# Performance work log

Hardware: AMD Instinct MI355X
Metric: run time of the kernel (lower is better)

Reference implementation:

```python
import jax, jax.numpy as jnp
import numpy as np

GROUPS = 32
EPS = 1e-5


def setup_inputs() -> dict:
    key = jax.random.key(0)
    ks = jax.random.split(key, 7)
    B, C, H, W = 16, 512, 32, 32
    return {
        "x": jax.random.normal(ks[0], (B, C, H, W), jnp.float32),
        "norm_w": jax.random.uniform(ks[1], (C,), jnp.float32, 0.5, 1.5),
        "norm_b": jax.random.normal(ks[2], (C,), jnp.float32) * 0.1,
        "qkv_w": jax.random.normal(ks[3], (3 * C, C), jnp.float32) * (C ** -0.5),
        "qkv_b": jax.random.normal(ks[4], (3 * C,), jnp.float32) * 0.01,
        "proj_w": jax.random.normal(ks[5], (C, C), jnp.float32) * (C ** -0.5),
        "proj_b": jax.random.normal(ks[6], (C,), jnp.float32) * 0.01,
        "num_heads": 8,
    }


def _group_norm(x, w, b):
    # x: (B, C, T); GroupNorm over (C//G, T) per group, per-channel affine
    B, C, T = x.shape
    xg = x.reshape(B, GROUPS, C // GROUPS, T)
    mean = jnp.mean(xg, axis=(2, 3), keepdims=True)
    var = jnp.var(xg, axis=(2, 3), keepdims=True)
    xn = ((xg - mean) * jax.lax.rsqrt(var + EPS)).reshape(B, C, T)
    return xn * w[None, :, None] + b[None, :, None]


def reference(x, norm_w, norm_b, qkv_w, qkv_b, proj_w, proj_b, num_heads):
    B, C, H, W = x.shape
    T = H * W
    xf = x.reshape(B, C, T)
    # qkv conv1x1: (B, 3C, T)
    qkv = jnp.einsum('oc,bct->bot', qkv_w, _group_norm(xf, norm_w, norm_b)) \
        + qkv_b[None, :, None]
    # split heads: (B*H, 3*hd, T) then chunk on channel dim
    BH = B * num_heads
    qkv = qkv.reshape(BH, 3 * C // num_heads, T)
    q, k, v = jnp.split(qkv, 3, axis=1)  # each (BH, hd, T)
    hd = C // num_heads
    scale = hd ** -0.25
    # scores (BH, T, T), softmax in fp32 then cast back (matches torch)
    scores = jnp.einsum('bct,bcs->bts', q * scale, k * scale)
    w = jax.nn.softmax(scores.astype(jnp.float32), axis=-1).astype(scores.dtype)
    h = jnp.einsum('bts,bcs->bct', w, v)  # (BH, hd, T)
    h = h.reshape(B, C, T)
    h = jnp.einsum('oc,bct->bot', proj_w, h) + proj_b[None, :, None]
    return (h + xf).reshape(B, C, H, W)
```

## Files before the change

kernel.cpp:

```cpp
#include <hip/hip_runtime.h>

typedef unsigned short u16;
typedef unsigned int u32;
typedef __bf16 bf16x8 __attribute__((ext_vector_type(8)));
typedef float f32x4 __attribute__((ext_vector_type(4)));
typedef float f32x16 __attribute__((ext_vector_type(16)));

#define SCALE_QK 0.35355339059327373f
#define LOG2E 1.4426950408889634f

__device__ __forceinline__ u16 f2bf(float f) {
  u32 u = __float_as_uint(f);
  u += 0x7FFFu + ((u >> 16) & 1u);
  return (u16)(u >> 16);
}

__device__ __forceinline__ void gload16(const u16* g, u16* l) {
  __builtin_amdgcn_global_load_lds((const __attribute__((address_space(1))) void*)g,
                                   (__attribute__((address_space(3))) void*)l, 16, 0, 0);
}

__device__ __forceinline__ int rswz(int r) { return (r & 7) ^ ((r >> 3) & 3); }

__global__ __launch_bounds__(256) void k_prep(const float* __restrict__ x,
                                              const float* __restrict__ nw,
                                              const float* __restrict__ nb,
                                              const float* __restrict__ qkvw_f,
                                              const float* __restrict__ projw_f,
                                              u16* __restrict__ gnt,
                                              u16* __restrict__ qkvw,
                                              u16* __restrict__ projw) {
  const int bid = blockIdx.x;
  const int tid = threadIdx.x;

  if (bid >= 512) {
    const float* src = (bid < 1280) ? qkvw_f : projw_f;
    u16* dst = (bid < 1280) ? qkvw : projw;
    const int i = (bid - ((bid < 1280) ? 512 : 1280)) * 256 + tid;
    float4 v = ((const float4*)src)[i];
    u32 lo = (u32)f2bf(v.x) | ((u32)f2bf(v.y) << 16);
    u32 hi = (u32)f2bf(v.z) | ((u32)f2bf(v.w) << 16);
    ((uint2*)dst)[i] = make_uint2(lo, hi);
    return;
  }

  const int b = bid >> 5;
  const int g = bid & 31;
  const float* xg = x + ((size_t)b * 512 + g * 16) * 1024;

  float s = 0.f, ss = 0.f;
#pragma unroll
  for (int it = 0; it < 16; ++it) {
    float4 v = ((const float4*)xg)[tid + it * 256];
    s += v.x + v.y + v.z + v.w;
    ss += v.x * v.x + v.y * v.y + v.z * v.z + v.w * v.w;
  }
#pragma unroll
  for (int off = 32; off >= 1; off >>= 1) {
    s += __shfl_xor(s, off);
    ss += __shfl_xor(ss, off);
  }
  __shared__ float red[8];
  const int wid = tid >> 6, lane = tid & 63;
  if (lane == 0) { red[wid] = s; red[4 + wid] = ss; }
  __syncthreads();
  const float mean = (red[0] + red[1] + red[2] + red[3]) * (1.f / 16384.f);
  const float ex2 = (red[4] + red[5] + red[6] + red[7]) * (1.f / 16384.f);
  const float rstd = rsqrtf(ex2 - mean * mean + 1e-5f);

  const int cp = (tid & 7) * 2, tt = tid >> 3;
  const int c0 = g * 16 + cp;
  const float wc0 = nw[c0] * rstd, bc0 = nb[c0] - mean * wc0;
  const float wc1 = nw[c0 + 1] * rstd, bc1 = nb[c0 + 1] - mean * wc1;
  const float* xc0 = xg + (size_t)cp * 1024;
  const float* xc1 = xc0 + 1024;
  u16* dst = gnt + (size_t)b * 1024 * 512 + c0;
#pragma unroll 8
  for (int t = tt; t < 1024; t += 32) {
    const u32 v0 = f2bf(xc0[t] * wc0 + bc0);
    const u32 v1 = f2bf(xc1[t] * wc1 + bc1);
    *(u32*)(dst + (size_t)t * 512) = v0 | (v1 << 16);
  }
}

template <int MODE>
__global__ __launch_bounds__(512) void k_gemm(const u16* __restrict__ A,
                                              const u16* __restrict__ Bw,
                                              const float* __restrict__ bias,
                                              u16* __restrict__ Qb, u16* __restrict__ Kb,
                                              u16* __restrict__ Vb,
                                              const float* __restrict__ xres,
                                              float* __restrict__ out) {
  __shared__ u16 smem[32768];
  u16* Asb = smem;
  u16* Bsb = smem + 16384;
  const int tid = threadIdx.x;
  const int lane = tid & 63, wid = tid >> 6;
  const int wr = wid >> 1, wc = wid & 1;
  const int fid = blockIdx.x;
  const int m0 = (fid & 127) * 128;
  const int n0 = (fid >> 7) * 128;
  const int l15 = lane & 15, l4 = lane >> 4;
  const f32x4 fzero = {0.f, 0.f, 0.f, 0.f};

  f32x4 acc[2][4];
#pragma unroll
  for (int i = 0; i < 2; ++i)
#pragma unroll
    for (int j = 0; j < 4; ++j) acc[i][j] = fzero;

  const int lrow = (tid & 63) >> 3;
  const int lchunk = tid & 7;

  auto stage = [&](int bi, int kt) {
#pragma unroll
    for (int rd = 0; rd < 2; ++rd) {
      const int rbase = wid * 8 + rd * 64;
      const int r = rbase + lrow;
      const int q = lchunk ^ (r & 7);
      gload16(A + ((size_t)(m0 + r) * 512 + kt * 64 + q * 8), Asb + bi * 8192 + rbase * 64);
      gload16(Bw + ((size_t)(n0 + r) * 512 + kt * 64 + q * 8), Bsb + bi * 8192 + rbase * 64);
    }
  };

  stage(0, 0);
  stage(1, 1);

  for (int kt = 0; kt < 8; ++kt) {
    if (kt < 7) {
      asm volatile("s_waitcnt vmcnt(4)" ::: "memory");
    } else {
      asm volatile("s_waitcnt vmcnt(0)" ::: "memory");
    }
    __builtin_amdgcn_s_barrier();
    const int buf = kt & 1;
#pragma unroll
    for (int ks = 0; ks < 2; ++ks) {
      bf16x8 af[2], bfr[4];
#pragma unroll
      for (int mi = 0; mi < 2; ++mi) {
        const int row = wr * 32 + mi * 16 + l15;
        af[mi] = *(const bf16x8*)&Asb[buf * 8192 + row * 64 + (((((ks << 2) + l4)) ^ (row & 7)) << 3)];
      }
#pragma unroll
      for (int ni = 0; ni < 4; ++ni) {
        const int row = wc * 64 + ni * 16 + l15;
        bfr[ni] = *(const bf16x8*)&Bsb[buf * 8192 + row * 64 + (((((ks << 2) + l4)) ^ (row & 7)) << 3)];
      }
#pragma unroll
      for (int mi = 0; mi < 2; ++mi)
#pragma unroll
        for (int ni = 0; ni < 4; ++ni)
          acc[mi][ni] = __builtin_amdgcn_mfma_f32_16x16x32_bf16(af[mi], bfr[ni], acc[mi][ni], 0, 0, 0);
    }
    asm volatile("s_waitcnt lgkmcnt(0)" ::: "memory");
    __builtin_amdgcn_sched_barrier(0);
    __builtin_amdgcn_s_barrier();
    if (kt < 6) stage(buf, kt + 2);
  }

  if (MODE == 0) {
    const int oseg = n0 + wc * 64;
    const int h = oseg / 192;
    const int typ = (oseg - h * 192) >> 6;
    const int b = m0 >> 10;
    const int bh = b * 8 + h;
    const int t0w = (m0 & 1023) + wr * 32;
    if (typ < 2) {
      const float sc = (typ == 0) ? (SCALE_QK * LOG2E) : SCALE_QK;
      u16* scr = smem + wid * 4096;
#pragma unroll
      for (int ni = 0; ni < 4; ++ni) {
        const int ol = ni * 16 + l15;
        const float bo = bias[oseg + ol];
#pragma unroll
        for (int mi = 0; mi < 2; ++mi) {
#pragma unroll
          for (int jj = 0; jj < 4; ++jj) {
            const int tl = mi * 16 + l4 * 4 + jj;
            scr[tl * 72 + ol] = f2bf((acc[mi][ni][jj] + bo) * sc);
          }
        }
      }
      asm volatile("s_waitcnt lgkmcnt(0)" ::: "memory");
      u16* qk = (typ == 0) ? Qb : Kb;
      const int tr = lane & 31;
#pragma unroll
      for (int i = 0; i < 4; ++i) {
        const int ch = (lane >> 5) * 4 + i;
        const uint4 v = *(const uint4*)&scr[tr * 72 + ch * 8];
        *(uint4*)(qk + (((size_t)bh * 1024 + t0w + tr) << 6) + ch * 8) = v;
      }
    } else {
#pragma unroll
      for (int ni = 0; ni < 4; ++ni) {
        const int ci = ni * 16 + l15;
        const float bo = bias[oseg + ci];
#pragma unroll
        for (int mi = 0; mi < 2; ++mi) {
          const int t0 = t0w + mi * 16 + l4 * 4;
          const u32 w0 = (u32)f2bf(acc[mi][ni][0] + bo) | ((u32)f2bf(acc[mi][ni][1] + bo) << 16);
          const u32 w1 = (u32)f2bf(acc[mi][ni][2] + bo) | ((u32)f2bf(acc[mi][ni][3] + bo) << 16);
          *(uint2*)(Vb + (((size_t)bh * 64 + ci) << 10) + t0) = make_uint2(w0, w1);
        }
      }
    }
  } else {
#pragma unroll
    for (int ni = 0; ni < 4; ++ni) {
      const int o = n0 + wc * 64 + ni * 16 + l15;
      const float bo = bias[o];
#pragma unroll
      for (int mi = 0; mi < 2; ++mi) {
        const int mrow = m0 + wr * 32 + mi * 16 + l4 * 4;
        const int b = mrow >> 10, t0 = mrow & 1023;
        const size_t base = ((size_t)b * 512 + o) * 1024 + t0;
        const float4 xr = *(const float4*)(xres + base);
        float4 ov;
        ov.x = acc[mi][ni][0] + bo + xr.x;
        ov.y = acc[mi][ni][1] + bo + xr.y;
        ov.z = acc[mi][ni][2] + bo + xr.z;
        ov.w = acc[mi][ni][3] + bo + xr.w;
        *(float4*)(out + base) = ov;
      }
    }
  }
}

__global__ __launch_bounds__(256) void k_attn(const u16* __restrict__ Qb,
                                              const u16* __restrict__ Kb,
                                              const u16* __restrict__ Vb,
                                              u16* __restrict__ ht) {
  __shared__ u16 Ks[3][64][64];
  __shared__ u16 Vs[3][64][64];
  const int tid = threadIdx.x;
  const int lane = tid & 63, wid = tid >> 6;
  const int l31 = lane & 31, hi = lane >> 5;
  const int fid = blockIdx.x;
  const int bh = fid & 127, qt = fid >> 7;
  const int b = bh >> 3, head = bh & 7;
  const int lrow = lane >> 3, lchunk = lane & 7;
  const int rsw = rswz(l31);

  bf16x8 qf0[4], qf1[4];
  {
    const u16* qp0 = Qb + (((size_t)bh * 1024 + qt * 256 + wid * 64 + l31) << 6) + hi * 8;
    const u16* qp1 = qp0 + (32 << 6);
#pragma unroll
    for (int kc = 0; kc < 4; ++kc) {
      qf0[kc] = *(const bf16x8*)(qp0 + kc * 16);
      qf1[kc] = *(const bf16x8*)(qp1 + kc * 16);
    }
  }

  bf16x8 onesf;
#pragma unroll
  for (int i = 0; i < 8; ++i) onesf[i] = (l31 == 0) ? (__bf16)1.0f : (__bf16)0.0f;

  f32x16 ZERO;
#pragma unroll
  for (int r = 0; r < 16; ++r) ZERO[r] = 0.f;

  f32x16 oacc[2][2], osum[2];
#pragma unroll
  for (int g = 0; g < 2; ++g)
#pragma unroll
    for (int r = 0; r < 16; ++r) { oacc[g][0][r] = 0.f; oacc[g][1][r] = 0.f; osum[g][r] = 0.f; }

  auto stageKV = [&](int bi, int st) {
    const int s0 = st * 64;
#pragma unroll
    for (int rd = 0; rd < 2; ++rd) {
      const int rbase = wid * 8 + rd * 32;
      const int r = rbase + lrow;
      const int q = lchunk ^ rswz(r);
      gload16(Kb + (((size_t)bh * 1024 + s0 + r) << 6) + q * 8, &Ks[bi][rbase][0]);
      gload16(Vb + (((size_t)bh * 64 + r) << 10) + s0 + q * 8, &Vs[bi][rbase][0]);
    }
  };

  stageKV(0, 0);
  stageKV(1, 1);

  int bufc = 0, bufs = 2;
  for (int st = 0; st < 16; ++st) {
    if (st < 15) {
      asm volatile("s_waitcnt vmcnt(4)" ::: "memory");
    } else {
      asm volatile("s_waitcnt vmcnt(0)" ::: "memory");
    }
    __builtin_amdgcn_s_barrier();
    if (st < 14) stageKV(bufs, st + 2);

#pragma unroll
    for (int cb = 0; cb < 2; ++cb) {
      f32x16 sacc0, sacc1;
      __builtin_amdgcn_s_setprio(1);
#pragma unroll
      for (int kc = 0; kc < 4; ++kc) {
        const int r = cb * 32 + l31;
        const bf16x8 kb = *(const bf16x8*)&Ks[bufc][r][((((kc << 1) | hi)) ^ rsw) << 3];
        if (kc == 0) {
          sacc0 = __builtin_amdgcn_mfma_f32_32x32x16_bf16(kb, qf0[kc], ZERO, 0, 0, 0);
          sacc1 = __builtin_amdgcn_mfma_f32_32x32x16_bf16(kb, qf1[kc], ZERO, 0, 0, 0);
        } else {
          sacc0 = __builtin_amdgcn_mfma_f32_32x32x16_bf16(kb, qf0[kc], sacc0, 0, 0, 0);
          sacc1 = __builtin_amdgcn_mfma_f32_32x32x16_bf16(kb, qf1[kc], sacc1, 0, 0, 0);
        }
      }
      __builtin_amdgcn_s_setprio(0);
      float p0[16], p1[16];
#pragma unroll
      for (int r = 0; r < 16; ++r) {
        asm("v_exp_f32 %0, %1" : "=v"(p0[r]) : "v"(sacc0[r]));
        asm("v_exp_f32 %0, %1" : "=v"(p1[r]) : "v"(sacc1[r]));
      }

#pragma unroll
      for (int ksl = 0; ksl < 2; ++ksl) {
        u32 A0, A1, B0, B1, C0, C1, D0, D1;
        asm("v_cvt_pk_bf16_f32 %0, %1, %2" : "=v"(A0) : "v"(p0[8 * ksl + 0]), "v"(p0[8 * ksl + 1]));
        asm("v_cvt_pk_bf16_f32 %0, %1, %2" : "=v"(A1) : "v"(p0[8 * ksl + 2]), "v"(p0[8 * ksl + 3]));
        asm("v_cvt_pk_bf16_f32 %0, %1, %2" : "=v"(B0) : "v"(p0[8 * ksl + 4]), "v"(p0[8 * ksl + 5]));
        asm("v_cvt_pk_bf16_f32 %0, %1, %2" : "=v"(B1) : "v"(p0[8 * ksl + 6]), "v"(p0[8 * ksl + 7]));
        asm volatile("v_permlane32_swap_b32 %0, %1" : "+v"(A0), "+v"(B0));
        asm volatile("v_permlane32_swap_b32 %0, %1" : "+v"(A1), "+v"(B1));
        asm("v_cvt_pk_bf16_f32 %0, %1, %2" : "=v"(C0) : "v"(p1[8 * ksl + 0]), "v"(p1[8 * ksl + 1]));
        asm("v_cvt_pk_bf16_f32 %0, %1, %2" : "=v"(C1) : "v"(p1[8 * ksl + 2]), "v"(p1[8 * ksl + 3]));
        asm("v_cvt_pk_bf16_f32 %0, %1, %2" : "=v"(D0) : "v"(p1[8 * ksl + 4]), "v"(p1[8 * ksl + 5]));
        asm("v_cvt_pk_bf16_f32 %0, %1, %2" : "=v"(D1) : "v"(p1[8 * ksl + 6]), "v"(p1[8 * ksl + 7]));
        asm volatile("v_permlane32_swap_b32 %0, %1" : "+v"(C0), "+v"(D0));
        asm volatile("v_permlane32_swap_b32 %0, %1" : "+v"(C1), "+v"(D1));
        union { u32 w[4]; bf16x8 v; } pa0, pa1;
        pa0.w[0] = A0; pa0.w[1] = A1; pa0.w[2] = B0; pa0.w[3] = B1;
        pa1.w[0] = C0; pa1.w[1] = C1; pa1.w[2] = D0; pa1.w[3] = D1;
        const int ks = cb * 2 + ksl;
        __builtin_amdgcn_s_setprio(1);
#pragma unroll
        for (int db = 0; db < 2; ++db) {
          const int r = db * 32 + l31;
          const bf16x8 vb = *(const bf16x8*)&Vs[bufc][r][((((ks << 1) | hi)) ^ rsw) << 3];
          oacc[0][db] = __builtin_amdgcn_mfma_f32_32x32x16_bf16(pa0.v, vb, oacc[0][db], 0, 0, 0);
          oacc[1][db] = __builtin_amdgcn_mfma_f32_32x32x16_bf16(pa1.v, vb, oacc[1][db], 0, 0, 0);
        }
        osum[0] = __builtin_amdgcn_mfma_f32_32x32x16_bf16(pa0.v, onesf, osum[0], 0, 0, 0);
        osum[1] = __builtin_amdgcn_mfma_f32_32x32x16_bf16(pa1.v, onesf, osum[1], 0, 0, 0);
        __builtin_amdgcn_s_setprio(0);
      }
    }

    bufc = (bufc == 2) ? 0 : bufc + 1;
    bufs = (bufs == 2) ? 0 : bufs + 1;
  }

#pragma unroll
  for (int g = 0; g < 2; ++g) {
    float inv[16];
#pragma unroll
    for (int r = 0; r < 16; ++r) {
      const float ls = __shfl(osum[g][r], lane & 32);
      inv[r] = __builtin_amdgcn_rcpf(ls);
    }
    const int tg = qt * 256 + wid * 64 + g * 32;
#pragma unroll
    for (int db = 0; db < 2; ++db) {
#pragma unroll
      for (int r = 0; r < 16; ++r) {
        const int t = tg + (r & 3) + 8 * (r >> 2) + 4 * hi;
        const int cg = head * 64 + db * 32 + l31;
        ht[((size_t)b * 1024 + t) * 512 + cg] = f2bf(oacc[g][db][r] * inv[r]);
      }
    }
  }
}

extern "C" void kernel_launch(void* const* d_in, const int* in_sizes, int n_in,
                              void* d_out, int out_size, void* d_ws, size_t ws_size,
                              hipStream_t stream) {
  const float* x = (const float*)d_in[0];
  const float* norm_w = (const float*)d_in[1];
  const float* norm_b = (const float*)d_in[2];
  const float* qkv_w = (const float*)d_in[3];
  const float* qkv_b = (const float*)d_in[4];
  const float* proj_w = (const float*)d_in[5];
  const float* proj_b = (const float*)d_in[6];
  float* out = (float*)d_out;

  char* ws = (char*)d_ws;
  u16* qkvw = (u16*)(ws + 0);
  u16* projw = (u16*)(ws + 1572864);
  u16* gnt = (u16*)(ws + 2097152);
  u16* Qb = (u16*)(ws + 18874368);
  u16* Kb = (u16*)(ws + 35651584);
  u16* Vb = (u16*)(ws + 52428800);
  u16* ht = (u16*)(ws + 69206016);

  k_prep<<<1536, 256, 0, stream>>>(x, norm_w, norm_b, qkv_w, proj_w, gnt, qkvw, projw);
  k_gemm<0><<<1536, 512, 0, stream>>>(gnt, qkvw, qkv_b, Qb, Kb, Vb, nullptr, nullptr);
  k_attn<<<512, 256, 0, stream>>>(Qb, Kb, Vb, ht);
  k_gemm<1><<<512, 512, 0, stream>>>(ht, projw, proj_b, nullptr, nullptr, nullptr, x, out);
}
```

Baseline: 135.7 us.

## Switch GEMMs to 32x32x16 MFMA with four 64x64-tile waves per block

The QKV and projection GEMM kernels go from 8 waves per block, each computing a 32x64 tile with 16x16x32 MFMAs, to 4 waves per block, each computing a 64x64 tile with 32x32x16 MFMAs. Staging now issues four async global-to-LDS loads per operand per thread with a new swizzle, and the wait count changes to match. The epilogues are rewritten for the 32x32 accumulator layout. Each wave does more MFMA work per LDS fragment load, which improves operand reuse, but there are half as many waves to hide latency and register pressure from the 16-wide accumulators goes up.

```diff
diff --git a/kernel.cpp b/kernel.cpp
--- a/kernel.cpp
+++ b/kernel.cpp
@@ -84,7 +84,7 @@
 }
 
 template <int MODE>
-__global__ __launch_bounds__(512) void k_gemm(const u16* __restrict__ A,
+__global__ __launch_bounds__(256) void k_gemm(const u16* __restrict__ A,
                                               const u16* __restrict__ Bw,
                                               const float* __restrict__ bias,
                                               u16* __restrict__ Qb, u16* __restrict__ Kb,
@@ -92,34 +92,34 @@
                                               const float* __restrict__ xres,
                                               float* __restrict__ out) {
   __shared__ u16 smem[32768];
-  u16* Asb = smem;
-  u16* Bsb = smem + 16384;
   const int tid = threadIdx.x;
   const int lane = tid & 63, wid = tid >> 6;
-  const int wr = wid >> 1, wc = wid & 1;
+  const int wm = wid >> 1, wn = wid & 1;
   const int fid = blockIdx.x;
   const int m0 = (fid & 127) * 128;
   const int n0 = (fid >> 7) * 128;
-  const int l15 = lane & 15, l4 = lane >> 4;
-  const f32x4 fzero = {0.f, 0.f, 0.f, 0.f};
-
-  f32x4 acc[2][4];
+  const int l31 = lane & 31, hi = lane >> 5;
+  const int rsw = rswz(l31);
+
+  f32x16 acc[2][2];
 #pragma unroll
   for (int i = 0; i < 2; ++i)
 #pragma unroll
-    for (int j = 0; j < 4; ++j) acc[i][j] = fzero;
-
-  const int lrow = (tid & 63) >> 3;
-  const int lchunk = tid & 7;
+    for (int j = 0; j < 2; ++j)
+#pragma unroll
+      for (int r = 0; r < 16; ++r) acc[i][j][r] = 0.f;
+
+  const int lr8 = lane >> 3, lc8 = lane & 7;
 
   auto stage = [&](int bi, int kt) {
-#pragma unroll
-    for (int rd = 0; rd < 2; ++rd) {
-      const int rbase = wid * 8 + rd * 64;
-      const int r = rbase + lrow;
-      const int q = lchunk ^ (r & 7);
-      gload16(A + ((size_t)(m0 + r) * 512 + kt * 64 + q * 8), Asb + bi * 8192 + rbase * 64);
-      gload16(Bw + ((size_t)(n0 + r) * 512 + kt * 64 + q * 8), Bsb + bi * 8192 + rbase * 64);
+    u16* ab = smem + bi * 8192 + wid * 512;
+    u16* bb = smem + 16384 + bi * 8192 + wid * 512;
+#pragma unroll
+    for (int i = 0; i < 4; ++i) {
+      const int r = wid * 8 + i * 32 + lr8;
+      const int c8 = lc8 ^ rswz(r);
+      gload16(A + ((size_t)(m0 + r) * 512 + kt * 64 + c8 * 8), ab + i * 2048);
+      gload16(Bw + ((size_t)(n0 + r) * 512 + kt * 64 + c8 * 8), bb + i * 2048);
     }
   };
 
@@ -128,30 +128,31 @@
 
   for (int kt = 0; kt < 8; ++kt) {
     if (kt < 7) {
-      asm volatile("s_waitcnt vmcnt(4)" ::: "memory");
+      asm volatile("s_waitcnt vmcnt(8)" ::: "memory");
     } else {
       asm volatile("s_waitcnt vmcnt(0)" ::: "memory");
     }
     __builtin_amdgcn_s_barrier();
     const int buf = kt & 1;
 #pragma unroll
-    for (int ks = 0; ks < 2; ++ks) {
-      bf16x8 af[2], bfr[4];
+    for (int kc = 0; kc < 4; ++kc) {
+      const int ch = kc * 2 + hi;
+      bf16x8 af[2], bfv[2];
 #pragma unroll
       for (int mi = 0; mi < 2; ++mi) {
-        const int row = wr * 32 + mi * 16 + l15;
-        af[mi] = *(const bf16x8*)&Asb[buf * 8192 + row * 64 + (((((ks << 2) + l4)) ^ (row & 7)) << 3)];
-      }
-#pragma unroll
-      for (int ni = 0; ni < 4; ++ni) {
-        const int row = wc * 64 + ni * 16 + l15;
-        bfr[ni] = *(const bf16x8*)&Bsb[buf * 8192 + row * 64 + (((((ks << 2) + l4)) ^ (row & 7)) << 3)];
+        const int row = wm * 64 + mi * 32 + l31;
+        af[mi] = *(const bf16x8*)&smem[buf * 8192 + row * 64 + ((ch ^ rsw) << 3)];
+      }
+#pragma unroll
+      for (int ni = 0; ni < 2; ++ni) {
+        const int row = wn * 64 + ni * 32 + l31;
+        bfv[ni] = *(const bf16x8*)&smem[16384 + buf * 8192 + row * 64 + ((ch ^ rsw) << 3)];
       }
 #pragma unroll
       for (int mi = 0; mi < 2; ++mi)
 #pragma unroll
-        for (int ni = 0; ni < 4; ++ni)
-          acc[mi][ni] = __builtin_amdgcn_mfma_f32_16x16x32_bf16(af[mi], bfr[ni], acc[mi][ni], 0, 0, 0);
+        for (int ni = 0; ni < 2; ++ni)
+          acc[mi][ni] = __builtin_amdgcn_mfma_f32_32x32x16_bf16(af[mi], bfv[ni], acc[mi][ni], 0, 0, 0);
     }
     asm volatile("s_waitcnt lgkmcnt(0)" ::: "memory");
     __builtin_amdgcn_sched_barrier(0);
@@ -159,69 +160,76 @@
     if (kt < 6) stage(buf, kt + 2);
   }
 
+  const int b = m0 >> 10;
   if (MODE == 0) {
-    const int oseg = n0 + wc * 64;
+    const int oseg = n0 + wn * 64;
     const int h = oseg / 192;
     const int typ = (oseg - h * 192) >> 6;
-    const int b = m0 >> 10;
     const int bh = b * 8 + h;
-    const int t0w = (m0 & 1023) + wr * 32;
+    const int t0w = (m0 & 1023) + wm * 64;
     if (typ < 2) {
       const float sc = (typ == 0) ? (SCALE_QK * LOG2E) : SCALE_QK;
-      u16* scr = smem + wid * 4096;
-#pragma unroll
-      for (int ni = 0; ni < 4; ++ni) {
-        const int ol = ni * 16 + l15;
+      u16* scr = smem + wid * 4608;
+#pragma unroll
+      for (int ni = 0; ni < 2; ++ni) {
+        const int ol = ni * 32 + l31;
         const float bo = bias[oseg + ol];
 #pragma unroll
         for (int mi = 0; mi < 2; ++mi) {
 #pragma unroll
-          for (int jj = 0; jj < 4; ++jj) {
-            const int tl = mi * 16 + l4 * 4 + jj;
-            scr[tl * 72 + ol] = f2bf((acc[mi][ni][jj] + bo) * sc);
+          for (int r = 0; r < 16; ++r) {
+            const int tl = mi * 32 + (r & 3) + 8 * (r >> 2) + 4 * hi;
+            scr[tl * 72 + ol] = f2bf((acc[mi][ni][r] + bo) * sc);
           }
         }
       }
       asm volatile("s_waitcnt lgkmcnt(0)" ::: "memory");
       u16* qk = (typ == 0) ? Qb : Kb;
-      const int tr = lane & 31;
-#pragma unroll
-      for (int i = 0; i < 4; ++i) {
-        const int ch = (lane >> 5) * 4 + i;
-        const uint4 v = *(const uint4*)&scr[tr * 72 + ch * 8];
-        *(uint4*)(qk + (((size_t)bh * 1024 + t0w + tr) << 6) + ch * 8) = v;
+      u16* dst = qk + (((size_t)bh * 1024 + t0w + lane) << 6);
+#pragma unroll
+      for (int i = 0; i < 8; ++i) {
+        const uint4 v = *(const uint4*)&scr[lane * 72 + i * 8];
+        *(uint4*)(dst + i * 8) = v;
       }
     } else {
 #pragma unroll
-      for (int ni = 0; ni < 4; ++ni) {
-        const int ci = ni * 16 + l15;
-        const float bo = bias[oseg + ci];
+      for (int ni = 0; ni < 2; ++ni) {
+        const int ci = ni * 32 + l31;
+        const float bo = bias[oseg + ni * 32 + l31];
+        u16* vrow = Vb + (((size_t)bh * 64 + ci) << 10);
 #pragma unroll
         for (int mi = 0; mi < 2; ++mi) {
-          const int t0 = t0w + mi * 16 + l4 * 4;
-          const u32 w0 = (u32)f2bf(acc[mi][ni][0] + bo) | ((u32)f2bf(acc[mi][ni][1] + bo) << 16);
-          const u32 w1 = (u32)f2bf(acc[mi][ni][2] + bo) | ((u32)f2bf(acc[mi][ni][3] + bo) << 16);
-          *(uint2*)(Vb + (((size_t)bh * 64 + ci) << 10) + t0) = make_uint2(w0, w1);
+#pragma unroll
+          for (int rq = 0; rq < 4; ++rq) {
+            const int t = t0w + mi * 32 + 8 * rq + 4 * hi;
+            const u32 w0 = (u32)f2bf(acc[mi][ni][rq * 4 + 0] + bo) |
+                           ((u32)f2bf(acc[mi][ni][rq * 4 + 1] + bo) << 16);
+            const u32 w1 = (u32)f2bf(acc[mi][ni][rq * 4 + 2] + bo) |
+                           ((u32)f2bf(acc[mi][ni][rq * 4 + 3] + bo) << 16);
+            *(uint2*)(vrow + t) = make_uint2(w0, w1);
+          }
         }
       }
     }
   } else {
 #pragma unroll
-    for (int ni = 0; ni < 4; ++ni) {
-      const int o = n0 + wc * 64 + ni * 16 + l15;
+    for (int ni = 0; ni < 2; ++ni) {
+      const int o = n0 + wn * 64 + ni * 32 + l31;
       const float bo = bias[o];
+      const size_t obase = ((size_t)b * 512 + o) * 1024;
 #pragma unroll
       for (int mi = 0; mi < 2; ++mi) {
-        const int mrow = m0 + wr * 32 + mi * 16 + l4 * 4;
-        const int b = mrow >> 10, t0 = mrow & 1023;
-        const size_t base = ((size_t)b * 512 + o) * 1024 + t0;
-        const float4 xr = *(const float4*)(xres + base);
-        float4 ov;
-        ov.x = acc[mi][ni][0] + bo + xr.x;
-        ov.y = acc[mi][ni][1] + bo + xr.y;
-        ov.z = acc[mi][ni][2] + bo + xr.z;
-        ov.w = acc[mi][ni][3] + bo + xr.w;
-        *(float4*)(out + base) = ov;
+#pragma unroll
+        for (int rq = 0; rq < 4; ++rq) {
+          const int t = (m0 & 1023) + wm * 64 + mi * 32 + 8 * rq + 4 * hi;
+          const float4 xr = *(const float4*)(xres + obase + t);
+          float4 ov;
+          ov.x = acc[mi][ni][rq * 4 + 0] + bo + xr.x;
+          ov.y = acc[mi][ni][rq * 4 + 1] + bo + xr.y;
+          ov.z = acc[mi][ni][rq * 4 + 2] + bo + xr.z;
+          ov.w = acc[mi][ni][rq * 4 + 3] + bo + xr.w;
+          *(float4*)(out + obase + t) = ov;
+        }
       }
     }
   }
@@ -396,7 +404,7 @@
   u16* ht = (u16*)(ws + 69206016);
 
   k_prep<<<1536, 256, 0, stream>>>(x, norm_w, norm_b, qkv_w, proj_w, gnt, qkvw, projw);
-  k_gemm<0><<<1536, 512, 0, stream>>>(gnt, qkvw, qkv_b, Qb, Kb, Vb, nullptr, nullptr);
+  k_gemm<0><<<1536, 256, 0, stream>>>(gnt, qkvw, qkv_b, Qb, Kb, Vb, nullptr, nullptr);
   k_attn<<<512, 256, 0, stream>>>(Qb, Kb, Vb, ht);
-  k_gemm<1><<<512, 512, 0, stream>>>(ht, projw, proj_b, nullptr, nullptr, nullptr, x, out);
-}
+  k_gemm<1><<<512, 256, 0, stream>>>(ht, projw, proj_b, nullptr, nullptr, nullptr, x, out);
+}
```

Result: slower. 139.5 us (+2.8%).
